# Performance work log

Hardware: AMD Instinct MI355X
Metric: run time of the kernel (lower is better)

Reference implementation:

```python
import jax, jax.numpy as jnp
import numpy as np

CHANNELS = 32


def _mlp(x, W1, b1, W2, b2, W3, b3):
    # FNN: Linear -> ReLU -> Linear -> ReLU -> Linear (last layer linear)
    h = jax.nn.relu(x @ W1 + b1)
    h = jax.nn.relu(h @ W2 + b2)
    return h @ W3 + b3


def setup_inputs() -> dict:
    key = jax.random.key(0)
    ks = jax.random.split(key, 8)
    E = 262144
    C = CHANNELS
    H = 128
    d_in = 4  # 2 * spatial_dim
    d_out = C * (C + 1)  # 1056
    s = lambda fan_in: 1.0 / np.sqrt(fan_in)
    return {
        "pos_i": jax.random.normal(ks[0], (E, 2), jnp.float32),
        "pos_j": jax.random.normal(ks[1], (E, 2), jnp.float32),
        "v_j": jax.random.normal(ks[2], (E, C), jnp.float32),
        "W1": jax.random.normal(ks[3], (d_in, H), jnp.float32) * s(d_in),
        "b1": jnp.zeros((H,), jnp.float32),
        "W2": jax.random.normal(ks[4], (H, H), jnp.float32) * s(H),
        "b2": jnp.zeros((H,), jnp.float32),
        "W3": jax.random.normal(ks[5], (H, d_out), jnp.float32) * s(H),
        "b3": jnp.zeros((d_out,), jnp.float32),
    }


def reference(pos_i, pos_j, v_j, W1, b1, W2, b2, W3, b3):
    C = CHANNELS
    pos_ij = jnp.concatenate((pos_i, pos_j), axis=-1)          # [E, 2*spatial_dim]
    kernel = _mlp(pos_ij, W1, b1, W2, b2, W3, b3)
    kernel = kernel.reshape(-1, C, C + 1)                      # [E, C, C+1]
    mat, bias = kernel[..., :, :-1], kernel[..., :, -1]        # [E,C,C], [E,C]
    return jnp.einsum('eij,ej->ei', mat, v_j) + bias           # [E, C]
```

## Files before the change

kernel.cpp:

```cpp
#include <hip/hip_runtime.h>


#define E_TOTAL 262144
#define EPB 256
#define NBLK (E_TOTAL / EPB)

typedef float f32x4 __attribute__((ext_vector_type(4)));
typedef short s8v  __attribute__((ext_vector_type(8)));

__device__ __forceinline__ unsigned short f2bf(float x) {
  unsigned u = __float_as_uint(x);
  u += 0x7fffu + ((u >> 16) & 1u);
  return (unsigned short)(u >> 16);
}

__global__ void prep_pack(const float* __restrict__ W2, const float* __restrict__ W3,
                          const float* __restrict__ b3,
                          unsigned short* __restrict__ Wg2, unsigned short* __restrict__ W2f,
                          unsigned short* __restrict__ b3f, float* __restrict__ b3c) {
  int idx = blockIdx.x * 256 + threadIdx.x;
  if (idx < 135168) {
    int jj = idx & 7, lane = (idx >> 3) & 63;
    int ksnn = idx >> 9, ks = ksnn & 3, nn = ksnn >> 2;
    int nnt = (nn < 33) ? (2 * nn) : (2 * (nn - 33) + 1);
    int k = ks * 32 + ((lane >> 4) << 3) + jj;
    int col = nnt * 16 + (lane & 15);
    int i = col & 31, j = col >> 5;
    Wg2[idx] = f2bf(W3[k * 1056 + i * 33 + j]);
  }
  if (idx < 16384) {
    int ks = idx >> 12, nt = (idx >> 9) & 7, l = (idx >> 3) & 63, jj = idx & 7;
    int k = ks * 32 + ((l >> 4) << 3) + jj;
    int n = nt * 16 + (l & 15);
    W2f[idx] = f2bf(W2[k * 128 + n]);
  }
  if (idx < 1024) {
    int jj = idx & 7, lane = (idx >> 3) & 63, ih = idx >> 9;
    int j = ((lane >> 4) << 3) + jj, i = ih * 16 + (lane & 15);
    b3f[idx] = f2bf(b3[i * 33 + j]);
  }
  if (idx < 32) b3c[idx] = b3[idx * 33 + 32];
}

__device__ __forceinline__ void tile_load(s8v (&dst)[4], const unsigned short* __restrict__ Wg2,
                                          int n, int lane) {
  const s8v* src = (const s8v*)(Wg2 + (size_t)n * 2048 + lane * 8);
#pragma unroll
  for (int ks = 0; ks < 4; ++ks) dst[ks] = src[ks * 64];
}

__device__ __forceinline__ void tile_compute(const s8v (&bf)[4], const float* __restrict__ vt,
                                             int j, int eoff,
                                             const s8v (&af)[4][4], float (&oa)[4][4]) {
  const f32x4 zero4 = {0.f, 0.f, 0.f, 0.f};
  const float* vp = vt + j * 260 + eoff;
#pragma unroll
  for (int m = 0; m < 4; ++m) {
    f32x4 vv = *(const f32x4*)(vp + m * 16);
    f32x4 p = __builtin_amdgcn_mfma_f32_16x16x32_bf16(af[m][0], bf[0], zero4, 0, 0, 0);
#pragma unroll
    for (int ks = 1; ks < 4; ++ks)
      p = __builtin_amdgcn_mfma_f32_16x16x32_bf16(af[m][ks], bf[ks], p, 0, 0, 0);
#pragma unroll
    for (int r = 0; r < 4; ++r) oa[m][r] += vv[r] * p[r];
  }
}

__device__ __forceinline__ void init_oa(float (&oa)[4][4], const float* __restrict__ vj,
                                        const unsigned short* __restrict__ b3f,
                                        const float* __restrict__ b3c,
                                        int B0, int w, int q, int ln, int lane, int ih) {
  s8v b3fr = *(const s8v*)(b3f + (ih * 64 + lane) * 8);
  float cbv = b3c[ih * 16 + ln];
  f32x4 ci = {cbv, cbv, cbv, cbv};
#pragma unroll
  for (int m = 0; m < 4; ++m) {
    int e = B0 + w * 64 + m * 16 + ln;
    const float4 va = *(const float4*)(vj + (size_t)e * 32 + q * 8);
    const float4 vb = *(const float4*)(vj + (size_t)e * 32 + q * 8 + 4);
    s8v t;
    t[0] = (short)f2bf(va.x); t[1] = (short)f2bf(va.y);
    t[2] = (short)f2bf(va.z); t[3] = (short)f2bf(va.w);
    t[4] = (short)f2bf(vb.x); t[5] = (short)f2bf(vb.y);
    t[6] = (short)f2bf(vb.z); t[7] = (short)f2bf(vb.w);
    f32x4 p = __builtin_amdgcn_mfma_f32_16x16x32_bf16(t, b3fr, ci, 0, 0, 0);
#pragma unroll
    for (int r = 0; r < 4; ++r) oa[m][r] = p[r];
  }
}

__device__ __forceinline__ void store_half(float* __restrict__ out, const float (&oa)[4][4],
                                           int B0, int w, int q, int ln, int ih) {
#pragma unroll
  for (int m = 0; m < 4; ++m)
#pragma unroll
    for (int r = 0; r < 4; ++r) {
      int e = B0 + w * 64 + m * 16 + q * 4 + r;
      out[(size_t)e * 32 + ih * 16 + ln] = oa[m][r];
    }
}

__global__ __launch_bounds__(256, 2) void fnn_fused(
    const float* __restrict__ pos_i, const float* __restrict__ pos_j,
    const float* __restrict__ vj, const float* __restrict__ W1,
    const float* __restrict__ b1, const float* __restrict__ b2,
    const unsigned short* __restrict__ W2f, const unsigned short* __restrict__ Wg2,
    const unsigned short* __restrict__ b3f, const float* __restrict__ b3c,
    float* __restrict__ out) {
  __shared__ __attribute__((aligned(16))) char smem[34320];
  float* vt = (float*)smem;
  unsigned short* h2n = (unsigned short*)smem;
  unsigned short* h1c = (unsigned short*)(smem + 17408);

  const int tid = threadIdx.x;
  const int w = tid >> 6, lane = tid & 63, q = lane >> 4, ln = lane & 15;
  const int B0 = blockIdx.x * EPB;
  const int eoff = w * 64 + q * 4;

  float oa[4][4];
  init_oa(oa, vj, b3f, b3c, B0, w, q, ln, lane, 0);

  const int hh0 = (tid & 15) * 8;
  float w1r[4][8], b1r[8];
#pragma unroll
  for (int d = 0; d < 4; ++d)
#pragma unroll
    for (int u = 0; u < 8; ++u) w1r[d][u] = W1[d * 128 + hh0 + u];
#pragma unroll
  for (int u = 0; u < 8; ++u) b1r[u] = b1[hh0 + u];

  s8v af[4][4];
  for (int qtr = 0; qtr < 4; ++qtr) {
    for (int cb = 0; cb < 2; ++cb) {
#pragma unroll
      for (int half = 0; half < 2; ++half) {
        int ee = (tid >> 4) + half * 16;
        int eg = B0 + qtr * 64 + cb * 32 + ee;
        float2 pi = *(const float2*)(pos_i + (size_t)eg * 2);
        float2 pj = *(const float2*)(pos_j + (size_t)eg * 2);
        s8v hv;
#pragma unroll
        for (int u = 0; u < 8; ++u) {
          float o = b1r[u] + pi.x * w1r[0][u] + pi.y * w1r[1][u] +
                    pj.x * w1r[2][u] + pj.y * w1r[3][u];
          hv[u] = (short)f2bf(fmaxf(o, 0.f));
        }
        *(s8v*)&h1c[ee * 136 + hh0] = hv;
      }
      __syncthreads();
#pragma unroll
      for (int s = 0; s < 4; ++s) {
        int tt = w * 4 + s, mt = tt >> 3, nt = tt & 7;
        f32x4 a4 = {0.f, 0.f, 0.f, 0.f};
#pragma unroll
        for (int ks = 0; ks < 4; ++ks) {
          s8v afr = *(const s8v*)&h1c[(mt * 16 + ln) * 136 + ks * 32 + q * 8];
          s8v bfr = *(const s8v*)(W2f + ((ks * 8 + nt) * 64 + lane) * 8);
          a4 = __builtin_amdgcn_mfma_f32_16x16x32_bf16(afr, bfr, a4, 0, 0, 0);
        }
        float b2v = b2[nt * 16 + ln];
        int eb = cb * 32 + mt * 16 + q * 4;
        int kc = nt * 16 + ln;
#pragma unroll
        for (int r = 0; r < 4; ++r)
          h2n[(eb + r) * 136 + kc] = f2bf(fmaxf(a4[r] + b2v, 0.f));
      }
      __syncthreads();
    }
    if (w == qtr) {
#pragma unroll
      for (int m = 0; m < 4; ++m)
#pragma unroll
        for (int ks = 0; ks < 4; ++ks)
          af[m][ks] = *(const s8v*)&h2n[(m * 16 + ln) * 136 + ks * 32 + q * 8];
    }
    __syncthreads();
  }

  s8v bfA[4], bfB[4];
  tile_load(bfA, Wg2, 0, lane);
  tile_load(bfB, Wg2, 1, lane);

  {
    const float* vrow = vj + (size_t)(B0 + tid) * 32;
#pragma unroll
    for (int j4 = 0; j4 < 8; ++j4) {
      float4 vv = *(const float4*)(vrow + j4 * 4);
      vt[(j4 * 4 + 0) * 260 + tid] = vv.x;
      vt[(j4 * 4 + 1) * 260 + tid] = vv.y;
      vt[(j4 * 4 + 2) * 260 + tid] = vv.z;
      vt[(j4 * 4 + 3) * 260 + tid] = vv.w;
    }
    vt[32 * 260 + tid] = 1.0f;
  }

#pragma unroll 1
  for (int c = 0; c < 16; ++c) {
    tile_compute(bfA, vt, 2 * c,     eoff, af, oa);
    tile_load(bfA, Wg2, 2 * c + 2, lane);
    tile_compute(bfB, vt, 2 * c + 1, eoff, af, oa);
    tile_load(bfB, Wg2, 2 * c + 3, lane);
  }
  tile_compute(bfA, vt, 32, eoff, af, oa);
  tile_load(bfA, Wg2, 34, lane);

  store_half(out, oa, B0, w, q, ln, 0);
  init_oa(oa, vj, b3f, b3c, B0, w, q, ln, lane, 1);

#pragma unroll 1
  for (int c = 0; c < 16; ++c) {
    tile_compute(bfB, vt, 2 * c,     eoff, af, oa);
    tile_load(bfB, Wg2, 35 + 2 * c, lane);
    tile_compute(bfA, vt, 2 * c + 1, eoff, af, oa);
    tile_load(bfA, Wg2, 36 + 2 * c, lane);
  }
  tile_compute(bfB, vt, 32, eoff, af, oa);
  store_half(out, oa, B0, w, q, ln, 1);
}

extern "C" void kernel_launch(void* const* d_in, const int* in_sizes, int n_in,
                              void* d_out, int out_size, void* d_ws, size_t ws_size,
                              hipStream_t stream) {
  const float* pos_i = (const float*)d_in[0];
  const float* pos_j = (const float*)d_in[1];
  const float* vj    = (const float*)d_in[2];
  const float* W1    = (const float*)d_in[3];
  const float* b1    = (const float*)d_in[4];
  const float* W2    = (const float*)d_in[5];
  const float* b2    = (const float*)d_in[6];
  const float* W3    = (const float*)d_in[7];
  const float* b3    = (const float*)d_in[8];
  float* outp = (float*)d_out;

  unsigned short* Wg2 = (unsigned short*)d_ws;
  unsigned short* W2f = (unsigned short*)((char*)d_ws + 270336);
  unsigned short* b3f = (unsigned short*)((char*)d_ws + 303104);
  float*          b3c = (float*)((char*)d_ws + 305152);

  prep_pack<<<528, 256, 0, stream>>>(W2, W3, b3, Wg2, W2f, b3f, b3c);
  fnn_fused<<<NBLK, 256, 0, stream>>>(pos_i, pos_j, vj, W1, b1, b2, W2f, Wg2, b3f, b3c, outp);
}
```

Baseline: 184.9 us.

## Interleave MFMA chains, single-buffer W3 tiles, coalesce prep writes

The weight-tile loop drops its double-buffered bfA/bfB registers and uses a single buffer, loading tile n+1 after computing tile n. Within each tile, the four independent MFMA accumulation chains are interleaved across m so consecutive MFMAs do not wait on each other's results. The prep kernel now reads W3/W2 in source order and scatters the writes, making the global reads coalesced. Single buffering frees registers but can expose global-load latency, because each tile's load now has to finish before the next tile's compute.

```diff
diff --git a/kernel.cpp b/kernel.cpp
--- a/kernel.cpp
+++ b/kernel.cpp
@@ -20,19 +20,25 @@
                           unsigned short* __restrict__ b3f, float* __restrict__ b3c) {
   int idx = blockIdx.x * 256 + threadIdx.x;
   if (idx < 135168) {
-    int jj = idx & 7, lane = (idx >> 3) & 63;
-    int ksnn = idx >> 9, ks = ksnn & 3, nn = ksnn >> 2;
-    int nnt = (nn < 33) ? (2 * nn) : (2 * (nn - 33) + 1);
-    int k = ks * 32 + ((lane >> 4) << 3) + jj;
-    int col = nnt * 16 + (lane & 15);
-    int i = col & 31, j = col >> 5;
-    Wg2[idx] = f2bf(W3[k * 1056 + i * 33 + j]);
+    int k = idx / 1056, c = idx % 1056;
+    int i = c / 33, jc = c % 33;
+    int col = jc * 32 + i;
+    int nnt = col >> 4, low = col & 15;
+    int nn = (nnt & 1) ? (33 + (nnt >> 1)) : (nnt >> 1);
+    int ks = k >> 5, kr = k & 31;
+    int lane = ((kr >> 3) << 4) + low;
+    int jj = k & 7;
+    int dst = ((nn * 4 + ks) * 64 + lane) * 8 + jj;
+    Wg2[dst] = f2bf(W3[idx]);
   }
   if (idx < 16384) {
-    int ks = idx >> 12, nt = (idx >> 9) & 7, l = (idx >> 3) & 63, jj = idx & 7;
-    int k = ks * 32 + ((l >> 4) << 3) + jj;
-    int n = nt * 16 + (l & 15);
-    W2f[idx] = f2bf(W2[k * 128 + n]);
+    int k = idx >> 7, n = idx & 127;
+    int ks = k >> 5, kr = k & 31;
+    int nt = n >> 4, low = n & 15;
+    int l = ((kr >> 3) << 4) + low;
+    int jj = k & 7;
+    int dst = ((ks * 8 + nt) * 64 + l) * 8 + jj;
+    W2f[dst] = f2bf(W2[idx]);
   }
   if (idx < 1024) {
     int jj = idx & 7, lane = (idx >> 3) & 63, ih = idx >> 9;
@@ -54,15 +60,20 @@
                                              const s8v (&af)[4][4], float (&oa)[4][4]) {
   const f32x4 zero4 = {0.f, 0.f, 0.f, 0.f};
   const float* vp = vt + j * 260 + eoff;
+  f32x4 p[4];
+#pragma unroll
+  for (int m = 0; m < 4; ++m)
+    p[m] = __builtin_amdgcn_mfma_f32_16x16x32_bf16(af[m][0], bf[0], zero4, 0, 0, 0);
+#pragma unroll
+  for (int ks = 1; ks < 4; ++ks)
+#pragma unroll
+    for (int m = 0; m < 4; ++m)
+      p[m] = __builtin_amdgcn_mfma_f32_16x16x32_bf16(af[m][ks], bf[ks], p[m], 0, 0, 0);
 #pragma unroll
   for (int m = 0; m < 4; ++m) {
     f32x4 vv = *(const f32x4*)(vp + m * 16);
-    f32x4 p = __builtin_amdgcn_mfma_f32_16x16x32_bf16(af[m][0], bf[0], zero4, 0, 0, 0);
-#pragma unroll
-    for (int ks = 1; ks < 4; ++ks)
-      p = __builtin_amdgcn_mfma_f32_16x16x32_bf16(af[m][ks], bf[ks], p, 0, 0, 0);
-#pragma unroll
-    for (int r = 0; r < 4; ++r) oa[m][r] += vv[r] * p[r];
+#pragma unroll
+    for (int r = 0; r < 4; ++r) oa[m][r] += vv[r] * p[m][r];
   }
 }
 
@@ -177,9 +188,8 @@
     __syncthreads();
   }
 
-  s8v bfA[4], bfB[4];
-  tile_load(bfA, Wg2, 0, lane);
-  tile_load(bfB, Wg2, 1, lane);
+  s8v bf[4];
+  tile_load(bf, Wg2, 0, lane);
 
   {
     const float* vrow = vj + (size_t)(B0 + tid) * 32;
@@ -195,26 +205,19 @@
   }
 
 #pragma unroll 1
-  for (int c = 0; c < 16; ++c) {
-    tile_compute(bfA, vt, 2 * c,     eoff, af, oa);
-    tile_load(bfA, Wg2, 2 * c + 2, lane);
-    tile_compute(bfB, vt, 2 * c + 1, eoff, af, oa);
-    tile_load(bfB, Wg2, 2 * c + 3, lane);
-  }
-  tile_compute(bfA, vt, 32, eoff, af, oa);
-  tile_load(bfA, Wg2, 34, lane);
+  for (int n = 0; n < 33; ++n) {
+    tile_compute(bf, vt, n, eoff, af, oa);
+    tile_load(bf, Wg2, n + 1, lane);
+  }
 
   store_half(out, oa, B0, w, q, ln, 0);
   init_oa(oa, vj, b3f, b3c, B0, w, q, ln, lane, 1);
 
 #pragma unroll 1
-  for (int c = 0; c < 16; ++c) {
-    tile_compute(bfB, vt, 2 * c,     eoff, af, oa);
-    tile_load(bfB, Wg2, 35 + 2 * c, lane);
-    tile_compute(bfA, vt, 2 * c + 1, eoff, af, oa);
-    tile_load(bfA, Wg2, 36 + 2 * c, lane);
-  }
-  tile_compute(bfB, vt, 32, eoff, af, oa);
+  for (int n = 33; n < 66; ++n) {
+    tile_compute(bf, vt, n - 33, eoff, af, oa);
+    tile_load(bf, Wg2, n + 1, lane);
+  }
   store_half(out, oa, B0, w, q, ln, 1);
 }
 
```

New measurement: 178.7 us. 1.03x faster.
